# Kernel tuning notes

Measured on AMD Instinct MI355X. Metric: run time of the kernel, lower is better.

## Reference

```python
import jax, jax.numpy as jnp
import numpy as np

B, S, D = 2, 2048, 2048          # batch, max_seq_len, hidden_dim_attention
G, HPG = 8, 4                    # n_head_groups, n_heads_per_group
H = G * HPG                      # total heads = 32
HD = D // H                      # head_dim = 64
KV = D // G                      # kv projection dim = 256
DFF = 5632                       # hidden_dim_feedforward
EPS = 1e-6
SCALE = 1.0 / (jnp.sqrt(jnp.float32(D // G)) + EPS)  # sqrt(attention_dim // n_head_groups) + eps


def setup_inputs() -> dict:
    key = jax.random.key(0)
    ks = jax.random.split(key, 12)
    s = lambda fan_in: 1.0 / np.sqrt(fan_in)
    return {
        "x": jax.random.normal(ks[0], (B, S, D), jnp.float32),
        "position_matrix": jax.random.uniform(ks[1], (2, 1, S, D), jnp.float32),
        "norm_attn_w": jnp.ones((D,), jnp.float32),
        "norm_ff_w": jnp.ones((D,), jnp.float32),
        "wq": jax.random.normal(ks[2], (D, D), jnp.float32) * s(D),
        "wk": jax.random.normal(ks[3], (KV, D), jnp.float32) * s(D),
        "wv": jax.random.normal(ks[4], (KV, D), jnp.float32) * s(D),
        "wo": jax.random.normal(ks[5], (D, D), jnp.float32) * s(D),
        "gate_w": jax.random.normal(ks[6], (DFF, D), jnp.float32) * s(D),
        "up_w": jax.random.normal(ks[7], (DFF, D), jnp.float32) * s(D),
        "down_w": jax.random.normal(ks[8], (DFF, D).__class__((D, DFF)), jnp.float32) * s(DFF),
    }


def rmsnorm(x, w):
    xf = x.astype(jnp.float32)
    n = xf / (jnp.sqrt(jnp.mean(xf * xf, axis=-1, keepdims=True) + EPS) + EPS)
    return n.astype(x.dtype) * w


def embed_position(x, pm):
    # faithful to source: rotated half times (cos + sin) tables (source multiplies _x by both)
    d = x.shape[-1]
    _x = jnp.concatenate((-x[..., d // 2:], x[..., :d // 2]), axis=-1)
    return (_x * pm[0][:, :, :d] + _x * pm[1][:, :, :d]).astype(x.dtype)


def block(x, position_matrix, norm_attn_w, norm_ff_w, wq, wk, wv, wo, gate_w, up_w, down_w):
    # ---- attention sublayer ----
    h = rmsnorm(x, norm_attn_w)
    xq = h @ wq.T                                   # [B,S,D]
    xk = h @ wk.T                                   # [B,S,KV]
    xv = h @ wv.T                                   # [B,S,KV]
    xq = embed_position(xq, position_matrix)
    xk = embed_position(xk, position_matrix)
    # GQA broadcast: each group's KV dims split into HPG heads of HD
    xk = jnp.broadcast_to(xk[:, :, None, :], (B, S, G, KV)).reshape(B, S, H, HD).transpose(0, 2, 1, 3)
    xv = jnp.broadcast_to(xv[:, :, None, :], (B, S, G, KV)).reshape(B, S, H, HD).transpose(0, 2, 1, 3)
    xq = xq.reshape(B, S, H, HD).transpose(0, 2, 1, 3)  # [B,H,S,HD]
    score = jnp.einsum("bhqd,bhkd->bhqk", xq, xk) * SCALE
    # source mask: strictly-upper triangle filled with 1e-10 (added, not -inf) -- faithful
    mask = jnp.triu(jnp.full((S, S), 1e-10, jnp.float32), k=1)
    score = score + mask
    e = jnp.exp(score.astype(jnp.float32))
    attn = (e / (jnp.sum(e, axis=-1, keepdims=True) + 1.0)).astype(xq.dtype)
    out = jnp.einsum("bhqk,bhkd->bhqd", attn, xv)
    out = out.transpose(0, 2, 1, 3).reshape(B, S, D) @ wo.T
    x = x + out
    # ---- feedforward sublayer (SwiGLU) ----
    h2 = rmsnorm(x, norm_ff_w)
    ff = (jax.nn.silu(h2 @ gate_w.T) * (h2 @ up_w.T)) @ down_w.T
    return x + ff


def reference(x, position_matrix, norm_attn_w, norm_ff_w, wq, wk, wv, wo, gate_w, up_w, down_w):
    return block(x, position_matrix, norm_attn_w, norm_ff_w, wq, wk, wv, wo, gate_w, up_w, down_w)
```

## Files before the change

### kernel.cpp

```cpp
#include <hip/hip_runtime.h>


typedef __attribute__((ext_vector_type(8))) __bf16 bf16x8;
typedef __attribute__((ext_vector_type(4))) __bf16 bf16x4;
typedef __attribute__((ext_vector_type(4))) float f32x4;

#define RR 4096
#define DD 2048
#define KVD 256
#define QKVN 2560
#define DFF 5632

static const size_t OFF_WQKV = 0;
static const size_t OFF_WO   = 10485760;
static const size_t OFF_WG   = 18874368;
static const size_t OFF_WU   = 41943040;
static const size_t OFF_WDN  = 65011712;
static const size_t OFF_H    = 88080384;
static const size_t OFF_QKV  = 104857600;
static const size_t OFF_Q    = 125829120;
static const size_t OFF_K    = 142606336;
static const size_t OFF_ACT  = 144703488;
static const size_t WS_NEED  = 190840832;

__device__ __forceinline__ void glds16(const __bf16* g, __bf16* s) {
  __builtin_amdgcn_global_load_lds(
      (const __attribute__((address_space(1))) unsigned int*)(const void*)g,
      (__attribute__((address_space(3))) unsigned int*)(void*)s, 16, 0, 0);
}

__global__ void cvt_kernel(const float* __restrict__ s, __bf16* __restrict__ d, int n4) {
  int i = blockIdx.x * 256 + threadIdx.x;
  if (i >= n4) return;
  float4 v = ((const float4*)s)[i];
  union { __bf16 b[4]; ushort4 u; } c;
  c.b[0] = (__bf16)v.x; c.b[1] = (__bf16)v.y; c.b[2] = (__bf16)v.z; c.b[3] = (__bf16)v.w;
  ((ushort4*)d)[i] = c.u;
}

__global__ __launch_bounds__(256)
void rmsnorm_kernel(const float* __restrict__ x, const float* __restrict__ w,
                    __bf16* __restrict__ out) {
  const int row = blockIdx.x, t = threadIdx.x;
  const float4* xr = (const float4*)(x + (size_t)row * DD);
  float4 a = xr[t], b = xr[t + 256];
  float s = a.x*a.x + a.y*a.y + a.z*a.z + a.w*a.w
          + b.x*b.x + b.y*b.y + b.z*b.z + b.w*b.w;
#pragma unroll
  for (int m = 1; m < 64; m <<= 1) s += __shfl_xor(s, m, 64);
  __shared__ float red[4];
  if ((t & 63) == 0) red[t >> 6] = s;
  __syncthreads();
  float tot = red[0] + red[1] + red[2] + red[3];
  float inv = 1.0f / (sqrtf(tot * (1.0f / 2048.0f) + 1e-6f) + 1e-6f);
  const float4* wr = (const float4*)w;
  float4 w0 = wr[t], w1 = wr[t + 256];
  __bf16* o = out + (size_t)row * DD;
  union { __bf16 bb[4]; ushort4 u; } c;
  c.bb[0] = (__bf16)(a.x*inv*w0.x); c.bb[1] = (__bf16)(a.y*inv*w0.y);
  c.bb[2] = (__bf16)(a.z*inv*w0.z); c.bb[3] = (__bf16)(a.w*inv*w0.w);
  ((ushort4*)o)[t] = c.u;
  c.bb[0] = (__bf16)(b.x*inv*w1.x); c.bb[1] = (__bf16)(b.y*inv*w1.y);
  c.bb[2] = (__bf16)(b.z*inv*w1.z); c.bb[3] = (__bf16)(b.w*inv*w1.w);
  ((ushort4*)o)[t + 256] = c.u;
}

template<int EPI>
__global__ __launch_bounds__(256)
void gemm_nt_kernel(const __bf16* __restrict__ A, const __bf16* __restrict__ Bm,
                    __bf16* Cb, const float* __restrict__ Res,
                    float* __restrict__ Cf, int M, int N, int K) {
  __shared__ __align__(16) __bf16 As[128 * 32];
  __shared__ __align__(16) __bf16 Bs[128 * 32];
  const int t = threadIdx.x;
  const int GM = M >> 7, GN = N >> 7;
  int m_t, n_t;
  if (GM == 32 && (GN & 3) == 0) {
    int lid = blockIdx.y * gridDim.x + blockIdx.x;
    int xcd = lid & 7, i = lid >> 3;
    int c = i >> 4, j = i & 15;
    m_t = xcd * 4 + (j & 3);
    n_t = c * 4 + (j >> 2);
  } else {
    m_t = blockIdx.y; n_t = blockIdx.x;
  }
  const int m0 = m_t * 128, n0 = n_t * 128;
  const int w = t >> 6, l = t & 63;
  const int wm = w & 1, wn = w >> 1;
  const int lm = l & 15, lq = l >> 4;
  const int slot = w * 64 + l;
  const int r0 = slot >> 2;
  const int a0 = slot & 3;
  const __bf16* Ap0 = A + (size_t)(m0 + r0) * K + a0 * 8;
  const __bf16* Ap1 = A + (size_t)(m0 + r0 + 64) * K + a0 * 8;
  const __bf16* Bp0 = Bm + (size_t)(n0 + r0) * K + a0 * 8;
  const __bf16* Bp1 = Bm + (size_t)(n0 + r0 + 64) * K + a0 * 8;
  __bf16* AsW0 = As + w * 512;
  __bf16* AsW1 = As + 2048 + w * 512;
  __bf16* BsW0 = Bs + w * 512;
  __bf16* BsW1 = Bs + 2048 + w * 512;
  f32x4 acc[4][4] = {};
  for (int kt = 0; kt < K; kt += 32) {
    __syncthreads();
    glds16(Ap0 + kt, AsW0);
    glds16(Ap1 + kt, AsW1);
    glds16(Bp0 + kt, BsW0);
    glds16(Bp1 + kt, BsW1);
    __syncthreads();
    bf16x8 af[4], bfr[4];
#pragma unroll
    for (int i = 0; i < 4; i++)
      af[i] = *(const bf16x8*)&As[(wm * 64 + i * 16 + lm) * 32 + lq * 8];
#pragma unroll
    for (int j = 0; j < 4; j++)
      bfr[j] = *(const bf16x8*)&Bs[(wn * 64 + j * 16 + lm) * 32 + lq * 8];
#pragma unroll
    for (int i = 0; i < 4; i++)
#pragma unroll
      for (int j = 0; j < 4; j++)
        acc[i][j] = __builtin_amdgcn_mfma_f32_16x16x32_bf16(af[i], bfr[j], acc[i][j], 0, 0, 0);
  }
#pragma unroll
  for (int i = 0; i < 4; i++)
#pragma unroll
    for (int j = 0; j < 4; j++)
#pragma unroll
      for (int r = 0; r < 4; r++) {
        int row = m0 + wm * 64 + i * 16 + lq * 4 + r;
        int col = n0 + wn * 64 + j * 16 + lm;
        size_t idx = (size_t)row * N + col;
        if (EPI == 0) {
          Cb[idx] = (__bf16)acc[i][j][r];
        } else if (EPI == 1) {
          Cf[idx] = Res[idx] + acc[i][j][r];
        } else {
          float g = (float)Cb[idx];
          Cb[idx] = (__bf16)(g / (1.0f + __expf(-g)) * acc[i][j][r]);
        }
      }
}

__global__ __launch_bounds__(256)
void rope_kernel(const __bf16* __restrict__ qkv, const float* __restrict__ pm,
                 __bf16* __restrict__ qo, __bf16* __restrict__ ko) {
  const int row = blockIdx.x, t = threadIdx.x;
  const int s = row & 2047;
  const __bf16* q = qkv + (size_t)row * QKVN;
  const float* p0 = pm + (size_t)s * DD;
  const float* p1 = p0 + (size_t)2048 * DD;
  __bf16* qr = qo + (size_t)row * DD;
#pragma unroll
  for (int jj = 0; jj < 8; jj++) {
    int i = t + jj * 256;
    float rot = (i < 1024) ? -(float)q[i + 1024] : (float)q[i - 1024];
    qr[i] = (__bf16)(rot * (p0[i] + p1[i]));
  }
  const __bf16* k = q + 2048;
  __bf16* kr = ko + (size_t)row * KVD;
  {
    int i = t;
    float rot = (i < 128) ? -(float)k[i + 128] : (float)k[i - 128];
    kr[i] = (__bf16)(rot * (p0[i] + p1[i]));
  }
}

__global__ __launch_bounds__(256)
void attn_kernel(const __bf16* __restrict__ Q, const __bf16* __restrict__ Kb,
                 const __bf16* __restrict__ QKV, __bf16* __restrict__ O) {
  __shared__ __align__(16) __bf16 sQ[128 * 72];
  __shared__ __align__(16) __bf16 sK[64 * 72];
  __shared__ __align__(16) __bf16 sV[64 * 72];
  __shared__ float sDen[128];
  const int t = threadIdx.x, l = t & 63, w = t >> 6;
  const int lm = l & 15, lq = l >> 4;
  const int q0 = blockIdx.x * 128;
  const int h = blockIdx.y, b = blockIdx.z;
  const int p = h & 3;
  const float scale = 1.0f / (16.0f + 1e-6f);
  {
    const int qr = t >> 3, qc = (t & 7) * 8;
#pragma unroll
    for (int it = 0; it < 4; it++) {
      size_t base = ((size_t)(b * 2048 + q0 + qr + it * 32)) * DD + h * 64 + qc;
      *(uint4*)&sQ[(qr + it * 32) * 72 + qc] = *(const uint4*)(Q + base);
    }
  }
  f32x4 oacc[2][4] = {};
  float dsum[2] = {0.f, 0.f};
  const int ksr = t >> 2, ksc = (t & 3) * 16;
  for (int kt = 0; kt < 2048; kt += 64) {
    const __bf16* krow = Kb + ((size_t)(b * 2048 + kt + ksr)) * KVD + p * 64 + ksc;
    uint4 kv0 = *(const uint4*)(krow);
    uint4 kv1 = *(const uint4*)(krow + 8);
    unsigned int vpack[8];
    {
      const __bf16* vbase = QKV + ((size_t)(b * 2048 + kt + w * 16)) * QKVN + 2304 + p * 64 + l;
#pragma unroll
      for (int j2 = 0; j2 < 8; j2++) {
        unsigned int u0 = *(const unsigned short*)(vbase + (size_t)(2 * j2) * QKVN);
        unsigned int u1 = *(const unsigned short*)(vbase + (size_t)(2 * j2 + 1) * QKVN);
        vpack[j2] = u0 | (u1 << 16);
      }
    }
    __syncthreads();
    *(uint4*)&sK[ksr * 72 + ksc] = kv0;
    *(uint4*)&sK[ksr * 72 + ksc + 8] = kv1;
    *(uint4*)&sV[l * 72 + w * 16] = *(uint4*)&vpack[0];
    *(uint4*)&sV[l * 72 + w * 16 + 8] = *(uint4*)&vpack[4];
    __syncthreads();
    bf16x8 bQ[2][2];
#pragma unroll
    for (int q_j = 0; q_j < 2; q_j++)
#pragma unroll
      for (int kk = 0; kk < 2; kk++)
        bQ[q_j][kk] = *(const bf16x8*)&sQ[(w * 32 + q_j * 16 + lm) * 72 + kk * 32 + lq * 8];
#pragma unroll
    for (int kt2 = 0; kt2 < 2; kt2++) {
      union { bf16x8 v; __bf16 e[8]; } pA[2];
#pragma unroll
      for (int c = 0; c < 2; c++) {
        const int kt_i = kt2 * 2 + c;
        f32x4 sacc[2] = {};
#pragma unroll
        for (int kk = 0; kk < 2; kk++) {
          bf16x8 aK = *(const bf16x8*)&sK[(kt_i * 16 + lm) * 72 + kk * 32 + lq * 8];
#pragma unroll
          for (int q_j = 0; q_j < 2; q_j++)
            sacc[q_j] = __builtin_amdgcn_mfma_f32_16x16x32_bf16(aK, bQ[q_j][kk], sacc[q_j], 0, 0, 0);
        }
#pragma unroll
        for (int q_j = 0; q_j < 2; q_j++)
#pragma unroll
          for (int r = 0; r < 4; r++) {
            float e = __expf(sacc[q_j][r] * scale);
            dsum[q_j] += e;
            pA[q_j].e[c * 4 + r] = (__bf16)e;
          }
      }
#pragma unroll
      for (int d_n = 0; d_n < 4; d_n++) {
        union { bf16x8 v; bf16x4 h[2]; } bV;
        const __bf16* vb = &sV[(d_n * 16 + lm) * 72 + kt2 * 32 + lq * 4];
        bV.h[0] = *(const bf16x4*)(vb);
        bV.h[1] = *(const bf16x4*)(vb + 16);
#pragma unroll
        for (int q_j = 0; q_j < 2; q_j++)
          oacc[q_j][d_n] = __builtin_amdgcn_mfma_f32_16x16x32_bf16(pA[q_j].v, bV.v, oacc[q_j][d_n], 0, 0, 0);
      }
    }
  }
#pragma unroll
  for (int q_j = 0; q_j < 2; q_j++) {
    dsum[q_j] += __shfl_xor(dsum[q_j], 16, 64);
    dsum[q_j] += __shfl_xor(dsum[q_j], 32, 64);
  }
  if (l < 16) {
    sDen[w * 32 + l] = dsum[0];
    sDen[w * 32 + 16 + l] = dsum[1];
  }
  __syncthreads();
#pragma unroll
  for (int q_j = 0; q_j < 2; q_j++)
#pragma unroll
    for (int d_n = 0; d_n < 4; d_n++)
#pragma unroll
      for (int r = 0; r < 4; r++) {
        int rloc = w * 32 + q_j * 16 + lq * 4 + r;
        int row = q0 + rloc;
        int col = h * 64 + d_n * 16 + lm;
        O[((size_t)(b * 2048 + row)) * DD + col] = (__bf16)(oacc[q_j][d_n][r] / (sDen[rloc] + 1.0f));
      }
}

extern "C" void kernel_launch(void* const* d_in, const int* in_sizes, int n_in,
                              void* d_out, int out_size, void* d_ws, size_t ws_size,
                              hipStream_t stream) {
  if (ws_size < WS_NEED) return;

  const float* x    = (const float*)d_in[0];
  const float* pm   = (const float*)d_in[1];
  const float* w_na = (const float*)d_in[2];
  const float* w_nf = (const float*)d_in[3];
  const float* wq   = (const float*)d_in[4];
  const float* wk   = (const float*)d_in[5];
  const float* wv   = (const float*)d_in[6];
  const float* wo   = (const float*)d_in[7];
  const float* wg   = (const float*)d_in[8];
  const float* wu   = (const float*)d_in[9];
  const float* wd   = (const float*)d_in[10];

  char* ws = (char*)d_ws;
  __bf16* wqkv_b = (__bf16*)(ws + OFF_WQKV);
  __bf16* wo_b   = (__bf16*)(ws + OFF_WO);
  __bf16* wg_b   = (__bf16*)(ws + OFF_WG);
  __bf16* wu_b   = (__bf16*)(ws + OFF_WU);
  __bf16* wdn_b  = (__bf16*)(ws + OFF_WDN);
  __bf16* h_b    = (__bf16*)(ws + OFF_H);
  __bf16* qkv_b  = (__bf16*)(ws + OFF_QKV);
  __bf16* q_b    = (__bf16*)(ws + OFF_Q);
  __bf16* k_b    = (__bf16*)(ws + OFF_K);
  __bf16* act_b  = (__bf16*)(ws + OFF_ACT);
  float*  x1     = (float*)d_out;

  cvt_kernel<<<4096, 256, 0, stream>>>(wq, wqkv_b, 1048576);
  cvt_kernel<<<512, 256, 0, stream>>>(wk, wqkv_b + (size_t)2048 * 2048, 131072);
  cvt_kernel<<<512, 256, 0, stream>>>(wv, wqkv_b + (size_t)2304 * 2048, 131072);
  cvt_kernel<<<4096, 256, 0, stream>>>(wo, wo_b, 1048576);
  cvt_kernel<<<11264, 256, 0, stream>>>(wg, wg_b, 2883584);
  cvt_kernel<<<11264, 256, 0, stream>>>(wu, wu_b, 2883584);
  cvt_kernel<<<11264, 256, 0, stream>>>(wd, wdn_b, 2883584);

  rmsnorm_kernel<<<4096, 256, 0, stream>>>(x, w_na, h_b);
  gemm_nt_kernel<0><<<dim3(20, 32), 256, 0, stream>>>(h_b, wqkv_b, qkv_b, nullptr, nullptr,
                                                      RR, QKVN, DD);
  rope_kernel<<<4096, 256, 0, stream>>>(qkv_b, pm, q_b, k_b);
  attn_kernel<<<dim3(16, 32, 2), 256, 0, stream>>>(q_b, k_b, qkv_b, h_b);
  gemm_nt_kernel<1><<<dim3(16, 32), 256, 0, stream>>>(h_b, wo_b, nullptr, x, x1,
                                                      RR, DD, DD);
  rmsnorm_kernel<<<4096, 256, 0, stream>>>(x1, w_nf, q_b);
  gemm_nt_kernel<0><<<dim3(44, 32), 256, 0, stream>>>(q_b, wg_b, act_b, nullptr, nullptr,
                                                      RR, DFF, DD);
  gemm_nt_kernel<2><<<dim3(44, 32), 256, 0, stream>>>(q_b, wu_b, act_b, nullptr, nullptr,
                                                      RR, DFF, DD);
  gemm_nt_kernel<1><<<dim3(16, 32), 256, 0, stream>>>(act_b, wdn_b, nullptr, x1, x1,
                                                      RR, DD, DFF);
}
```

Baseline: 987.7 us.

## Replace GEMM with 256x256 double-buffered swizzled-LDS kernel using 8 waves

Replaces the 128x128, BK=32, single-buffered GEMM with a 256x256 tile, BK=64 kernel using 512 threads. It double-buffers LDS with staggered global-to-LDS loads interleaved between MFMA clusters, XOR-swizzles the LDS layout to avoid bank conflicts, and raises MFMA priority with setprio. It also remaps workgroups across XCDs. The aim is to raise arithmetic intensity and hide load latency in the projection and FFN GEMMs. In exchange it uses much more LDS (128KB per block) and fewer blocks, which risks poor occupancy and wave quantization on the N=2048 GEMMs (128 tiles on 256 CUs).

```diff
diff --git a/kernel.cpp b/kernel.cpp
--- a/kernel.cpp
+++ b/kernel.cpp
@@ -66,67 +66,97 @@
 }
 
 template<int EPI>
-__global__ __launch_bounds__(256)
-void gemm_nt_kernel(const __bf16* __restrict__ A, const __bf16* __restrict__ Bm,
+__global__ __launch_bounds__(512, 2)
+void gemm256_kernel(const __bf16* __restrict__ A, const __bf16* __restrict__ Bm,
                     __bf16* Cb, const float* __restrict__ Res,
                     float* __restrict__ Cf, int M, int N, int K) {
-  __shared__ __align__(16) __bf16 As[128 * 32];
-  __shared__ __align__(16) __bf16 Bs[128 * 32];
-  const int t = threadIdx.x;
-  const int GM = M >> 7, GN = N >> 7;
-  int m_t, n_t;
-  if (GM == 32 && (GN & 3) == 0) {
-    int lid = blockIdx.y * gridDim.x + blockIdx.x;
-    int xcd = lid & 7, i = lid >> 3;
-    int c = i >> 4, j = i & 15;
-    m_t = xcd * 4 + (j & 3);
-    n_t = c * 4 + (j >> 2);
-  } else {
-    m_t = blockIdx.y; n_t = blockIdx.x;
-  }
-  const int m0 = m_t * 128, n0 = n_t * 128;
-  const int w = t >> 6, l = t & 63;
+  __shared__ __align__(16) __bf16 LA[2][256 * 64];
+  __shared__ __align__(16) __bf16 LB[2][256 * 64];
+  const int t = threadIdx.x, w = t >> 6, l = t & 63;
+  const int lm = l & 15, lq = l >> 4;
   const int wm = w & 1, wn = w >> 1;
-  const int lm = l & 15, lq = l >> 4;
-  const int slot = w * 64 + l;
-  const int r0 = slot >> 2;
-  const int a0 = slot & 3;
-  const __bf16* Ap0 = A + (size_t)(m0 + r0) * K + a0 * 8;
-  const __bf16* Ap1 = A + (size_t)(m0 + r0 + 64) * K + a0 * 8;
-  const __bf16* Bp0 = Bm + (size_t)(n0 + r0) * K + a0 * 8;
-  const __bf16* Bp1 = Bm + (size_t)(n0 + r0 + 64) * K + a0 * 8;
-  __bf16* AsW0 = As + w * 512;
-  __bf16* AsW1 = As + 2048 + w * 512;
-  __bf16* BsW0 = Bs + w * 512;
-  __bf16* BsW1 = Bs + 2048 + w * 512;
-  f32x4 acc[4][4] = {};
-  for (int kt = 0; kt < K; kt += 32) {
-    __syncthreads();
-    glds16(Ap0 + kt, AsW0);
-    glds16(Ap1 + kt, AsW1);
-    glds16(Bp0 + kt, BsW0);
-    glds16(Bp1 + kt, BsW1);
-    __syncthreads();
-    bf16x8 af[4], bfr[4];
-#pragma unroll
-    for (int i = 0; i < 4; i++)
-      af[i] = *(const bf16x8*)&As[(wm * 64 + i * 16 + lm) * 32 + lq * 8];
+  const int NT = K >> 6;
+  const int nwg = gridDim.x * gridDim.y;
+  const int lid = blockIdx.y * gridDim.x + blockIdx.x;
+  const int q8 = nwg >> 3, r8 = nwg & 7;
+  const int xcd = lid & 7, j0 = lid >> 3;
+  const int wg = (xcd < r8 ? xcd * (q8 + 1) : r8 * (q8 + 1) + (xcd - r8) * q8) + j0;
+  const int GN = N >> 8;
+  const int m0 = (wg / GN) << 8, n0 = (wg % GN) << 8;
+
+  const int srow = l >> 3, sslot = (l & 7) ^ srow;
+  const __bf16* Ag = A + (size_t)(m0 + w * 8 + srow) * K + sslot * 8;
+  const __bf16* Bg = Bm + (size_t)(n0 + w * 8 + srow) * K + sslot * 8;
+  const int dstoff = w * 8 * 64;
+
+  const int aRow = (wm * 128 + lm) * 64;
+  const int bRow = (wn * 64 + lm) * 64;
+  const int sl0 = ((lq) ^ (lm & 7)) << 3;
+  const int sl1 = ((4 + lq) ^ (lm & 7)) << 3;
+
+  f32x4 acc[8][4] = {};
+  bf16x8 aa[4], bb[4];
+
+#define ST_A(bufi, kti, c) glds16(Ag + (size_t)((c) * 64) * K + (size_t)(kti) * 64, \
+                                  &LA[bufi][(c) * 4096 + dstoff])
+#define ST_B(bufi, kti, c) glds16(Bg + (size_t)((c) * 64) * K + (size_t)(kti) * 64, \
+                                  &LB[bufi][(c) * 4096 + dstoff])
+#define RD_A(i, kkslot) *(const bf16x8*)&LA[buf][aRow + (i) * 1024 + (kkslot)]
+#define RD_B(j, kkslot) *(const bf16x8*)&LB[buf][bRow + (j) * 1024 + (kkslot)]
+#define CLUSTER16(I0)                                                              \
+  __builtin_amdgcn_s_setprio(1);                                                   \
+  _Pragma("unroll") for (int jj = 0; jj < 4; ++jj) {                               \
+    acc[(I0) + 0][jj] = __builtin_amdgcn_mfma_f32_16x16x32_bf16(aa[0], bb[jj], acc[(I0) + 0][jj], 0, 0, 0); \
+    acc[(I0) + 1][jj] = __builtin_amdgcn_mfma_f32_16x16x32_bf16(aa[1], bb[jj], acc[(I0) + 1][jj], 0, 0, 0); \
+    acc[(I0) + 2][jj] = __builtin_amdgcn_mfma_f32_16x16x32_bf16(aa[2], bb[jj], acc[(I0) + 2][jj], 0, 0, 0); \
+    acc[(I0) + 3][jj] = __builtin_amdgcn_mfma_f32_16x16x32_bf16(aa[3], bb[jj], acc[(I0) + 3][jj], 0, 0, 0); \
+  }                                                                                \
+  __builtin_amdgcn_s_setprio(0);
+#define BAR() do { __builtin_amdgcn_s_barrier(); asm volatile("" ::: "memory"); } while (0)
+
+  ST_A(0, 0, 0); ST_A(0, 0, 1); ST_A(0, 0, 2); ST_A(0, 0, 3);
+  ST_B(0, 0, 0); ST_B(0, 0, 1); ST_B(0, 0, 2); ST_B(0, 0, 3);
+  ST_A(1, 1, 0); ST_A(1, 1, 1);
+  asm volatile("s_waitcnt vmcnt(2)" ::: "memory");
+  __builtin_amdgcn_s_barrier();
+
+  for (int kt = 0; kt < NT; ++kt) {
+    const int buf = kt & 1, nb = buf ^ 1;
+    aa[0] = RD_A(0, sl0); aa[1] = RD_A(1, sl0); aa[2] = RD_A(2, sl0); aa[3] = RD_A(3, sl0);
+    bb[0] = RD_B(0, sl0); bb[1] = RD_B(1, sl0); bb[2] = RD_B(2, sl0); bb[3] = RD_B(3, sl0);
+    if (kt + 1 < NT) { ST_A(nb, kt + 1, 2); ST_A(nb, kt + 1, 3); }
+    BAR();
+    CLUSTER16(0);
+    BAR();
+    aa[0] = RD_A(4, sl0); aa[1] = RD_A(5, sl0); aa[2] = RD_A(6, sl0); aa[3] = RD_A(7, sl0);
+    if (kt + 1 < NT) { ST_B(nb, kt + 1, 0); ST_B(nb, kt + 1, 1); }
+    BAR();
+    CLUSTER16(4);
+    BAR();
+    aa[0] = RD_A(0, sl1); aa[1] = RD_A(1, sl1); aa[2] = RD_A(2, sl1); aa[3] = RD_A(3, sl1);
+    bb[0] = RD_B(0, sl1); bb[1] = RD_B(1, sl1); bb[2] = RD_B(2, sl1); bb[3] = RD_B(3, sl1);
+    if (kt + 1 < NT) { ST_B(nb, kt + 1, 2); ST_B(nb, kt + 1, 3); }
+    BAR();
+    CLUSTER16(0);
+    BAR();
+    aa[0] = RD_A(4, sl1); aa[1] = RD_A(5, sl1); aa[2] = RD_A(6, sl1); aa[3] = RD_A(7, sl1);
+    if (kt + 2 < NT) { ST_A(buf, kt + 2, 0); ST_A(buf, kt + 2, 1); }
+    BAR();
+    CLUSTER16(4);
+    if (kt + 1 < NT) {
+      if (kt + 2 < NT) asm volatile("s_waitcnt vmcnt(2)" ::: "memory");
+      else             asm volatile("s_waitcnt vmcnt(0)" ::: "memory");
+    }
+    BAR();
+  }
+
+#pragma unroll
+  for (int i = 0; i < 8; i++)
 #pragma unroll
     for (int j = 0; j < 4; j++)
-      bfr[j] = *(const bf16x8*)&Bs[(wn * 64 + j * 16 + lm) * 32 + lq * 8];
-#pragma unroll
-    for (int i = 0; i < 4; i++)
-#pragma unroll
-      for (int j = 0; j < 4; j++)
-        acc[i][j] = __builtin_amdgcn_mfma_f32_16x16x32_bf16(af[i], bfr[j], acc[i][j], 0, 0, 0);
-  }
-#pragma unroll
-  for (int i = 0; i < 4; i++)
-#pragma unroll
-    for (int j = 0; j < 4; j++)
 #pragma unroll
       for (int r = 0; r < 4; r++) {
-        int row = m0 + wm * 64 + i * 16 + lq * 4 + r;
+        int row = m0 + wm * 128 + i * 16 + lq * 4 + r;
         int col = n0 + wn * 64 + j * 16 + lm;
         size_t idx = (size_t)row * N + col;
         if (EPI == 0) {
@@ -138,6 +168,12 @@
           Cb[idx] = (__bf16)(g / (1.0f + __expf(-g)) * acc[i][j][r]);
         }
       }
+#undef ST_A
+#undef ST_B
+#undef RD_A
+#undef RD_B
+#undef CLUSTER16
+#undef BAR
 }
 
 __global__ __launch_bounds__(256)
@@ -311,17 +347,17 @@
   cvt_kernel<<<11264, 256, 0, stream>>>(wd, wdn_b, 2883584);
 
   rmsnorm_kernel<<<4096, 256, 0, stream>>>(x, w_na, h_b);
-  gemm_nt_kernel<0><<<dim3(20, 32), 256, 0, stream>>>(h_b, wqkv_b, qkv_b, nullptr, nullptr,
+  gemm256_kernel<0><<<dim3(10, 16), 512, 0, stream>>>(h_b, wqkv_b, qkv_b, nullptr, nullptr,
                                                       RR, QKVN, DD);
   rope_kernel<<<4096, 256, 0, stream>>>(qkv_b, pm, q_b, k_b);
   attn_kernel<<<dim3(16, 32, 2), 256, 0, stream>>>(q_b, k_b, qkv_b, h_b);
-  gemm_nt_kernel<1><<<dim3(16, 32), 256, 0, stream>>>(h_b, wo_b, nullptr, x, x1,
-                                                      RR, DD, DD);
+  gemm256_kernel<1><<<dim3(8, 16), 512, 0, stream>>>(h_b, wo_b, nullptr, x, x1,
+                                                     RR, DD, DD);
   rmsnorm_kernel<<<4096, 256, 0, stream>>>(x1, w_nf, q_b);
-  gemm_nt_kernel<0><<<dim3(44, 32), 256, 0, stream>>>(q_b, wg_b, act_b, nullptr, nullptr,
+  gemm256_kernel<0><<<dim3(22, 16), 512, 0, stream>>>(q_b, wg_b, act_b, nullptr, nullptr,
                                                       RR, DFF, DD);
-  gemm_nt_kernel<2><<<dim3(44, 32), 256, 0, stream>>>(q_b, wu_b, act_b, nullptr, nullptr,
+  gemm256_kernel<2><<<dim3(22, 16), 512, 0, stream>>>(q_b, wu_b, act_b, nullptr, nullptr,
                                                       RR, DFF, DD);
-  gemm_nt_kernel<1><<<dim3(16, 32), 256, 0, stream>>>(act_b, wdn_b, nullptr, x1, x1,
-                                                      RR, DD, DFF);
-}
+  gemm256_kernel<1><<<dim3(8, 16), 512, 0, stream>>>(act_b, wdn_b, nullptr, x1, x1,
+                                                     RR, DD, DFF);
+}
```

Measured after the change: 1.010 ms. 1.02x slower.

## Add 128x256-tile 512-thread GEMM with XCD remap for O-proj and FFN

Applied to the files above, without the earlier changes.

Adds a new GEMM kernel with 128x256 output tiles, 8 waves per block, double-buffered LDS with direct global-to-LDS loads that are staged across two half-iterations, MFMA priority bumps, and a block-index remap that spreads tiles across the 8 XCDs. The output projection, gate, up and down GEMMs switch to it. Larger N tiles increase A reuse and cut global traffic per FLOP, and interleaving loads with MFMA clusters aims to hide memory latency. The cost is heavier LDS use and more barriers per K-step. Correctness depends on grid sizes dividing by 8 (256 and 704 do).

```diff
diff --git a/kernel.cpp b/kernel.cpp
--- a/kernel.cpp
+++ b/kernel.cpp
@@ -140,6 +140,102 @@
       }
 }
 
+template<int EPI>
+__global__ __launch_bounds__(512, 2)
+void gemm_nt2_kernel(const __bf16* __restrict__ A, const __bf16* __restrict__ Bm,
+                     __bf16* Cb, const float* __restrict__ Res,
+                     float* __restrict__ Cf, int M, int N, int K) {
+  __shared__ __align__(16) __bf16 LA[2][128 * 64];
+  __shared__ __align__(16) __bf16 LB[2][256 * 64];
+  const int t = threadIdx.x, w = t >> 6, l = t & 63;
+  const int lm = l & 15, lq = l >> 4;
+  const int wm = w >> 2, wn = w & 3;
+  const int NT = K >> 6;
+  const int nwg = gridDim.x * gridDim.y;
+  const int lid = blockIdx.y * gridDim.x + blockIdx.x;
+  const int q8 = nwg >> 3;
+  const int wg = (lid & 7) * q8 + (lid >> 3);
+  const int GN = N >> 8;
+  const int m0 = (wg / GN) << 7, n0 = (wg % GN) << 8;
+
+  const int srow = l >> 3, sslot = (l & 7) ^ srow;
+  const __bf16* Ag = A + (size_t)(m0 + w * 8 + srow) * K + sslot * 8;
+  const __bf16* Bg = Bm + (size_t)(n0 + w * 8 + srow) * K + sslot * 8;
+  const int dstoff = w * 512;
+
+  const int sl0 = ((lq) ^ (lm & 7)) << 3;
+  const int sl1 = ((4 + lq) ^ (lm & 7)) << 3;
+  const int aRow = (wm * 64 + lm) * 64;
+  const int bRow = (wn * 64 + lm) * 64;
+
+  f32x4 acc[4][4] = {};
+  bf16x8 af[4], bf[4];
+
+#define ST_A(bufi, kti, c) glds16(Ag + (size_t)((c) * 64) * K + (size_t)(kti) * 64, \
+                                  &LA[bufi][(c) * 4096 + dstoff])
+#define ST_B(bufi, kti, c) glds16(Bg + (size_t)((c) * 64) * K + (size_t)(kti) * 64, \
+                                  &LB[bufi][(c) * 4096 + dstoff])
+#define BAR() do { __builtin_amdgcn_s_barrier(); asm volatile("" ::: "memory"); } while (0)
+#define CLUSTER16()                                                                \
+  __builtin_amdgcn_s_setprio(1);                                                   \
+  _Pragma("unroll") for (int jj = 0; jj < 4; ++jj) {                               \
+    acc[0][jj] = __builtin_amdgcn_mfma_f32_16x16x32_bf16(af[0], bf[jj], acc[0][jj], 0, 0, 0); \
+    acc[1][jj] = __builtin_amdgcn_mfma_f32_16x16x32_bf16(af[1], bf[jj], acc[1][jj], 0, 0, 0); \
+    acc[2][jj] = __builtin_amdgcn_mfma_f32_16x16x32_bf16(af[2], bf[jj], acc[2][jj], 0, 0, 0); \
+    acc[3][jj] = __builtin_amdgcn_mfma_f32_16x16x32_bf16(af[3], bf[jj], acc[3][jj], 0, 0, 0); \
+  }                                                                                \
+  __builtin_amdgcn_s_setprio(0);
+
+  ST_A(0, 0, 0); ST_A(0, 0, 1);
+  ST_B(0, 0, 0); ST_B(0, 0, 1); ST_B(0, 0, 2); ST_B(0, 0, 3);
+  asm volatile("s_waitcnt vmcnt(0)" ::: "memory");
+  __builtin_amdgcn_s_barrier();
+
+  for (int kt = 0; kt < NT; ++kt) {
+    const int buf = kt & 1, nb = buf ^ 1;
+#pragma unroll
+    for (int i = 0; i < 4; i++) af[i] = *(const bf16x8*)&LA[buf][aRow + i * 1024 + sl0];
+#pragma unroll
+    for (int j = 0; j < 4; j++) bf[j] = *(const bf16x8*)&LB[buf][bRow + j * 1024 + sl0];
+    if (kt + 1 < NT) { ST_B(nb, kt + 1, 0); ST_B(nb, kt + 1, 1); ST_B(nb, kt + 1, 2); }
+    BAR();
+    CLUSTER16();
+    BAR();
+#pragma unroll
+    for (int i = 0; i < 4; i++) af[i] = *(const bf16x8*)&LA[buf][aRow + i * 1024 + sl1];
+#pragma unroll
+    for (int j = 0; j < 4; j++) bf[j] = *(const bf16x8*)&LB[buf][bRow + j * 1024 + sl1];
+    if (kt + 1 < NT) { ST_B(nb, kt + 1, 3); ST_A(nb, kt + 1, 0); ST_A(nb, kt + 1, 1); }
+    BAR();
+    CLUSTER16();
+    if (kt + 1 < NT) asm volatile("s_waitcnt vmcnt(0)" ::: "memory");
+    BAR();
+  }
+
+#pragma unroll
+  for (int i = 0; i < 4; i++)
+#pragma unroll
+    for (int j = 0; j < 4; j++)
+#pragma unroll
+      for (int r = 0; r < 4; r++) {
+        int row = m0 + wm * 64 + i * 16 + lq * 4 + r;
+        int col = n0 + wn * 64 + j * 16 + lm;
+        size_t idx = (size_t)row * N + col;
+        if (EPI == 0) {
+          Cb[idx] = (__bf16)acc[i][j][r];
+        } else if (EPI == 1) {
+          Cf[idx] = Res[idx] + acc[i][j][r];
+        } else {
+          float g = (float)Cb[idx];
+          Cb[idx] = (__bf16)(g / (1.0f + __expf(-g)) * acc[i][j][r]);
+        }
+      }
+#undef ST_A
+#undef ST_B
+#undef BAR
+#undef CLUSTER16
+}
+
 __global__ __launch_bounds__(256)
 void rope_kernel(const __bf16* __restrict__ qkv, const float* __restrict__ pm,
                  __bf16* __restrict__ qo, __bf16* __restrict__ ko) {
@@ -315,13 +411,13 @@
                                                       RR, QKVN, DD);
   rope_kernel<<<4096, 256, 0, stream>>>(qkv_b, pm, q_b, k_b);
   attn_kernel<<<dim3(16, 32, 2), 256, 0, stream>>>(q_b, k_b, qkv_b, h_b);
-  gemm_nt_kernel<1><<<dim3(16, 32), 256, 0, stream>>>(h_b, wo_b, nullptr, x, x1,
+  gemm_nt2_kernel<1><<<dim3(8, 32), 512, 0, stream>>>(h_b, wo_b, nullptr, x, x1,
                                                       RR, DD, DD);
   rmsnorm_kernel<<<4096, 256, 0, stream>>>(x1, w_nf, q_b);
-  gemm_nt_kernel<0><<<dim3(44, 32), 256, 0, stream>>>(q_b, wg_b, act_b, nullptr, nullptr,
-                                                      RR, DFF, DD);
-  gemm_nt_kernel<2><<<dim3(44, 32), 256, 0, stream>>>(q_b, wu_b, act_b, nullptr, nullptr,
-                                                      RR, DFF, DD);
-  gemm_nt_kernel<1><<<dim3(16, 32), 256, 0, stream>>>(act_b, wdn_b, nullptr, x1, x1,
+  gemm_nt2_kernel<0><<<dim3(22, 32), 512, 0, stream>>>(q_b, wg_b, act_b, nullptr, nullptr,
+                                                       RR, DFF, DD);
+  gemm_nt2_kernel<2><<<dim3(22, 32), 512, 0, stream>>>(q_b, wu_b, act_b, nullptr, nullptr,
+                                                       RR, DFF, DD);
+  gemm_nt2_kernel<1><<<dim3(8, 32), 512, 0, stream>>>(act_b, wdn_b, nullptr, x1, x1,
                                                       RR, DD, DFF);
 }
```

Result: faster. 967.3 us (-2.1%).
